# Kernel tuning notes

Hardware: AMD Instinct MI355X
Metric: run time of the kernel (lower is better)

Reference implementation:

```python
import jax, jax.numpy as jnp
import numpy as np

B, N, E = 16, 1024, 32768
HEADS, OC = 4, 8          # GATConv: out_channels = d_out // heads = 8
D_IN, A_DIM = 33, 8
DM, DO = 16, 32
EPS_LN = 1e-5


def setup_inputs() -> dict:
    key = jax.random.key(0)
    ks = jax.random.split(key, 24)
    r = lambda k, s: (0.1 * jax.random.normal(k, s)).astype(jnp.float32)
    return {
        "H": jax.random.normal(ks[0], (B, N, D_IN + A_DIM + 1), dtype=jnp.float32),
        "edge_index": jax.random.randint(ks[1], (2, E), 0, N, dtype=jnp.int32),
        "fc_s_w": r(ks[2], (DM, D_IN)), "fc_s_b": r(ks[3], (DM,)),
        "fc_a_w": r(ks[4], (DM, A_DIM)), "fc_a_b": r(ks[5], (DM,)),
        "fc_r_w": r(ks[6], (DM, 1)), "fc_r_b": r(ks[7], (DM,)),
        "fuse_q": r(ks[8], (3, DM)),
        "fuse_k_w": r(ks[9], (DM, DM)),
        "fuse_v_w": r(ks[10], (DM, DM)),
        "proj_w": r(ks[11], (DO, DM)), "proj_b": r(ks[12], (DO,)),
        "post_w": r(ks[13], (DO, DO)), "post_b": r(ks[14], (DO,)),
        "ln_g": jnp.ones((DO,), jnp.float32), "ln_b": jnp.zeros((DO,), jnp.float32),
        "gat_w": r(ks[15], (HEADS * OC, DO)),
        "att_src": r(ks[16], (HEADS, OC)),
        "att_dst": r(ks[17], (HEADS, OC)),
        "gat_b": r(ks[18], (HEADS * OC,)),
    }


def reference(H, edge_index, fc_s_w, fc_s_b, fc_a_w, fc_a_b, fc_r_w, fc_r_b,
              fuse_q, fuse_k_w, fuse_v_w, proj_w, proj_b, post_w, post_b,
              ln_g, ln_b, gat_w, att_src, att_dst, gat_b):
    # ---- ObsEmbedding: split obs | prev-action | prev-reward, embed to DM ----
    s = H[..., :D_IN]
    a = H[..., D_IN:D_IN + A_DIM]
    rr = H[..., D_IN + A_DIM:]
    tok = jnp.stack([s @ fc_s_w.T + fc_s_b,
                     a @ fc_a_w.T + fc_a_b,
                     rr @ fc_r_w.T + fc_r_b], axis=-2)            # [B,N,3,DM]
    K = tok @ fuse_k_w.T
    V = tok @ fuse_v_w.T
    attn = jnp.einsum('qd,bntd->bnqt', fuse_q, K) / jnp.sqrt(jnp.float32(DM))
    w = jax.nn.softmax(attn, axis=-1)                             # [B,N,3,3]
    fused = jnp.einsum('bnqt,bntd->bnqd', w, V).mean(-2)          # [B,N,DM]
    z = jax.nn.relu(fused) @ proj_w.T + proj_b                    # [B,N,DO]
    h = jax.nn.relu(z @ post_w.T + post_b)
    mu = h.mean(-1, keepdims=True)
    var = ((h - mu) ** 2).mean(-1, keepdims=True)
    Hn = (h - mu) / jnp.sqrt(var + EPS_LN) * ln_g + ln_b          # [B,N,DO]

    # ---- GATConv (eval mode: dropout off, add_self_loops=False) ----
    src, dst = edge_index[0], edge_index[1]
    x = (Hn @ gat_w.T).reshape(B, N, HEADS, OC)                   # [B,N,H,OC]
    a_s = (x * att_src).sum(-1)                                   # [B,N,H]
    a_d = (x * att_dst).sum(-1)
    e = jax.nn.leaky_relu(a_s[:, src] + a_d[:, dst], 0.2)         # [B,E,H]

    def per_graph(e_b, x_b):
        # scatter-softmax over incoming edges of each destination node
        m = jax.ops.segment_max(e_b, dst, num_segments=N)
        ex = jnp.exp(e_b - m[dst])
        den = jax.ops.segment_sum(ex, dst, num_segments=N)
        alpha = ex / den[dst]                                     # [E,H]
        out = jax.ops.segment_sum(alpha[:, :, None] * x_b[src], dst,
                                  num_segments=N)                 # [N,H,OC]
        A = jnp.zeros((HEADS, N, N), jnp.float32).at[:, src, dst].add(alpha.T)
        A = A / jnp.maximum(A.sum(-1, keepdims=True), 1e-9)
        return out.reshape(N, HEADS * OC) + gat_b, A

    out, A = jax.vmap(per_graph)(e, x)                            # [B,N,32], [B,H,N,N]
    return out, A
```

## Files before the change

kernel.cpp:

```cpp
#include <hip/hip_runtime.h>
#include <math.h>

namespace {

constexpr int B = 16, N = 1024, E = 32768, HEADS = 4, OC = 8;
constexpr int D_IN = 33, A_DIM = 8, DM = 16, DO = 32;
constexpr int F = D_IN + A_DIM + 1;
constexpr int BCAP = 256;
constexpr int FILLB = E / 256;
constexpr int ROWS_PER_BLK = 8;

typedef float f4 __attribute__((ext_vector_type(4)));
typedef float f2 __attribute__((ext_vector_type(2)));

__device__ __forceinline__ float lrelu(float x) { return x >= 0.f ? x : 0.2f * x; }


__global__ __launch_bounds__(256) void k_prep(
    const int* __restrict__ ei, int* __restrict__ cnt_src,
    int* __restrict__ cnt_dst, int* __restrict__ bkt_src,
    int* __restrict__ bkt_dst,
    const float* __restrict__ H,
    const float* __restrict__ fc_s_w, const float* __restrict__ fc_s_b,
    const float* __restrict__ fc_a_w, const float* __restrict__ fc_a_b,
    const float* __restrict__ fc_r_w, const float* __restrict__ fc_r_b,
    const float* __restrict__ fuse_q, const float* __restrict__ fuse_k_w,
    const float* __restrict__ fuse_v_w, const float* __restrict__ proj_w,
    const float* __restrict__ proj_b, const float* __restrict__ post_w,
    const float* __restrict__ post_b, const float* __restrict__ ln_g,
    const float* __restrict__ ln_b, const float* __restrict__ gat_w,
    const float* __restrict__ att_src, const float* __restrict__ att_dst,
    float* __restrict__ x_out, float* __restrict__ as_out, float* __restrict__ advi) {
  if (blockIdx.x < FILLB) {
    int e = blockIdx.x * 256 + threadIdx.x;
    int s = ei[e], d = ei[E + e];
    int p1 = atomicAdd(&cnt_src[s], 1);
    if (p1 < BCAP) bkt_src[s * BCAP + p1] = d;
    int p2 = atomicAdd(&cnt_dst[d], 1);
    if (p2 < BCAP) bkt_dst[d * BCAP + p2] = s;
    return;
  }
  int node = (blockIdx.x - FILLB) * 256 + threadIdx.x;
  if (node >= B * N) return;

  const float* hin = H + (size_t)node * F;
  float hv[F];
#pragma unroll
  for (int i = 0; i < F; i++) hv[i] = hin[i];

  float tok[3][DM];
#pragma unroll
  for (int j = 0; j < DM; j++) {
    float acc = fc_s_b[j];
#pragma unroll
    for (int i = 0; i < D_IN; i++) acc = fmaf(hv[i], fc_s_w[j * D_IN + i], acc);
    tok[0][j] = acc;
    float acc2 = fc_a_b[j];
#pragma unroll
    for (int i = 0; i < A_DIM; i++) acc2 = fmaf(hv[D_IN + i], fc_a_w[j * A_DIM + i], acc2);
    tok[1][j] = acc2;
    tok[2][j] = fmaf(hv[F - 1], fc_r_w[j], fc_r_b[j]);
  }

  float Kf[3][DM], Vf[3][DM];
#pragma unroll
  for (int t = 0; t < 3; t++) {
#pragma unroll
    for (int j = 0; j < DM; j++) {
      float ak = 0.f, av = 0.f;
#pragma unroll
      for (int d = 0; d < DM; d++) {
        ak = fmaf(tok[t][d], fuse_k_w[j * DM + d], ak);
        av = fmaf(tok[t][d], fuse_v_w[j * DM + d], av);
      }
      Kf[t][j] = ak; Vf[t][j] = av;
    }
  }

  float wbar[3] = {0.f, 0.f, 0.f};
#pragma unroll
  for (int q = 0; q < 3; q++) {
    float att[3];
#pragma unroll
    for (int t = 0; t < 3; t++) {
      float acc = 0.f;
#pragma unroll
      for (int d = 0; d < DM; d++) acc = fmaf(fuse_q[q * DM + d], Kf[t][d], acc);
      att[t] = acc * 0.25f;
    }
    float mx = fmaxf(att[0], fmaxf(att[1], att[2]));
    float e0 = expf(att[0] - mx), e1 = expf(att[1] - mx), e2 = expf(att[2] - mx);
    float inv = 1.f / (e0 + e1 + e2);
    wbar[0] += e0 * inv; wbar[1] += e1 * inv; wbar[2] += e2 * inv;
  }

  float fused[DM];
#pragma unroll
  for (int d = 0; d < DM; d++) {
    float f = (wbar[0] * Vf[0][d] + wbar[1] * Vf[1][d] + wbar[2] * Vf[2][d]) * (1.f / 3.f);
    fused[d] = fmaxf(f, 0.f);
  }

  float z[DO];
#pragma unroll
  for (int o = 0; o < DO; o++) {
    float acc = proj_b[o];
#pragma unroll
    for (int d = 0; d < DM; d++) acc = fmaf(fused[d], proj_w[o * DM + d], acc);
    z[o] = acc;
  }

  float h2[DO]; float mu = 0.f;
#pragma unroll
  for (int o = 0; o < DO; o++) {
    float acc = post_b[o];
#pragma unroll
    for (int d = 0; d < DO; d++) acc = fmaf(z[d], post_w[o * DO + d], acc);
    acc = fmaxf(acc, 0.f);
    h2[o] = acc; mu += acc;
  }
  mu *= (1.f / DO);
  float var = 0.f;
#pragma unroll
  for (int o = 0; o < DO; o++) { float dd = h2[o] - mu; var = fmaf(dd, dd, var); }
  var *= (1.f / DO);
  float rstd = rsqrtf(var + 1e-5f);
  float Hn[DO];
#pragma unroll
  for (int o = 0; o < DO; o++) Hn[o] = fmaf((h2[o] - mu) * rstd, ln_g[o], ln_b[o]);

  float* xrow = x_out + (size_t)node * (HEADS * OC);
  f4 asv;
#pragma unroll
  for (int hh = 0; hh < HEADS; hh++) {
    float as = 0.f, ad = 0.f;
#pragma unroll
    for (int oc = 0; oc < OC; oc++) {
      int k = hh * OC + oc;
      float acc = 0.f;
#pragma unroll
      for (int d = 0; d < DO; d++) acc = fmaf(Hn[d], gat_w[k * DO + d], acc);
      xrow[k] = acc;
      as = fmaf(acc, att_src[k], as);
      ad = fmaf(acc, att_dst[k], ad);
    }
    asv[hh] = as;
    advi[(size_t)node * 8 + 2 * hh] = ad;
  }
  *(f4*)(as_out + (size_t)node * HEADS) = asv;
}

__global__ __launch_bounds__(256) void k_inv(
    const int* __restrict__ cnt_dst, const int* __restrict__ bkt_dst,
    const float* __restrict__ as_, float* __restrict__ advi) {
  int w = threadIdx.x >> 6, lane = threadIdx.x & 63;
  int r = blockIdx.x * 4 + w;
  int b = r & (B - 1), dn = r >> 4;
  int deg = min(cnt_dst[dn], BCAP);
  const int* list = bkt_dst + dn * BCAP;

  const float* adp = advi + (size_t)(b * N + dn) * 8;
  float a0 = adp[0], a1 = adp[2], a2 = adp[4], a3 = adp[6];

  float sm0 = 0.f, sm1 = 0.f, sm2 = 0.f, sm3 = 0.f;
  for (int i = lane; i < deg; i += 64) {
    int s = list[i];
    f4 ap = *(const f4*)(as_ + (size_t)(b * N + s) * HEADS);
    sm0 += __expf(lrelu(ap.x + a0));
    sm1 += __expf(lrelu(ap.y + a1));
    sm2 += __expf(lrelu(ap.z + a2));
    sm3 += __expf(lrelu(ap.w + a3));
  }
#pragma unroll
  for (int off = 1; off < 64; off <<= 1) {
    sm0 += __shfl_xor(sm0, off);
    sm1 += __shfl_xor(sm1, off);
    sm2 += __shfl_xor(sm2, off);
    sm3 += __shfl_xor(sm3, off);
  }
  if (lane == 0) {
    float* ivp = advi + (size_t)(b * N + dn) * 8 + 1;
    ivp[0] = sm0 > 0.f ? 1.f / sm0 : 0.f;
    ivp[2] = sm1 > 0.f ? 1.f / sm1 : 0.f;
    ivp[4] = sm2 > 0.f ? 1.f / sm2 : 0.f;
    ivp[6] = sm3 > 0.f ? 1.f / sm3 : 0.f;
  }
}

__global__ __launch_bounds__(256) void k_outA(
    const int* __restrict__ cnt_src, const int* __restrict__ bkt_src,
    const int* __restrict__ cnt_dst, const int* __restrict__ bkt_dst,
    const float* __restrict__ as_, const float* __restrict__ advi,
    const float* __restrict__ x_, const float* __restrict__ gat_b,
    float* __restrict__ out, float* __restrict__ A) {
  __shared__ float row[HEADS][N];
  int h = threadIdx.x >> 6, lane = threadIdx.x & 63;
  f4* rowv = (f4*)row[h];

  int r0 = blockIdx.x * ROWS_PER_BLK;
  int s = r0 >> 4;
  int degO = min(cnt_src[s], BCAP);
  const int* listO = bkt_src + s * BCAP;
  int degI = min(cnt_dst[s], BCAP);
  const int* listI = bkt_dst + s * BCAP;
  float gb = gat_b[h * OC + (lane & 7)];

  for (int r = r0; r < r0 + ROWS_PER_BLK; ++r) {
    int b = r & (B - 1);

#pragma unroll
    for (int j = 0; j < 4; j++) rowv[lane + j * 64] = (f4){0.f, 0.f, 0.f, 0.f};
    __syncthreads();

    float as_h = as_[(size_t)(b * N + s) * HEADS + h];
    float rs = 0.f;
    for (int i = lane; i < degO; i += 64) {
      int d = listO[i];
      f2 rec = *(const f2*)(advi + (size_t)(b * N + d) * 8 + 2 * h);
      float a = __expf(lrelu(as_h + rec.x)) * rec.y;
      atomicAdd(&row[h][d], a);
      rs += a;
    }
#pragma unroll
    for (int off = 1; off < 64; off <<= 1) rs += __shfl_xor(rs, off);

    {
      f2 self = *(const f2*)(advi + (size_t)(b * N + s) * 8 + 2 * h);
      int eslot = lane >> 3, cl = lane & 7, c = h * OC + cl;
      float acc = 0.f;
      for (int i = eslot; i < degI; i += 8) {
        int src = listI[i];
        float ex = __expf(lrelu(as_[(size_t)(b * N + src) * HEADS + h] + self.x));
        acc = fmaf(ex, x_[(size_t)(b * N + src) * (HEADS * OC) + c], acc);
      }
      acc += __shfl_xor(acc, 8);
      acc += __shfl_xor(acc, 16);
      acc += __shfl_xor(acc, 32);
      if (eslot == 0)
        out[(size_t)(b * N + s) * (HEADS * OC) + c] = acc * self.y + gb;
    }

    __syncthreads();

    float ivr = 1.f / fmaxf(rs, 1e-9f);
    float* Arow = A + (((size_t)b * HEADS + h) * N + s) * N;
#pragma unroll
    for (int j = 0; j < 4; j++) {
      f4 v = rowv[lane + j * 64];
      v.x *= ivr; v.y *= ivr; v.z *= ivr; v.w *= ivr;
      __builtin_nontemporal_store(v, (f4*)Arow + lane + j * 64);
    }
  }
}

}

extern "C" void kernel_launch(void* const* d_in, const int* in_sizes, int n_in,
                              void* d_out, int out_size, void* d_ws, size_t ws_size,
                              hipStream_t stream) {
  const float* H      = (const float*)d_in[0];
  const int*   ei     = (const int*)  d_in[1];
  const float* fc_s_w = (const float*)d_in[2];
  const float* fc_s_b = (const float*)d_in[3];
  const float* fc_a_w = (const float*)d_in[4];
  const float* fc_a_b = (const float*)d_in[5];
  const float* fc_r_w = (const float*)d_in[6];
  const float* fc_r_b = (const float*)d_in[7];
  const float* fuse_q = (const float*)d_in[8];
  const float* fuse_k_w = (const float*)d_in[9];
  const float* fuse_v_w = (const float*)d_in[10];
  const float* proj_w = (const float*)d_in[11];
  const float* proj_b = (const float*)d_in[12];
  const float* post_w = (const float*)d_in[13];
  const float* post_b = (const float*)d_in[14];
  const float* ln_g   = (const float*)d_in[15];
  const float* ln_b   = (const float*)d_in[16];
  const float* gat_w  = (const float*)d_in[17];
  const float* att_src = (const float*)d_in[18];
  const float* att_dst = (const float*)d_in[19];
  const float* gat_b  = (const float*)d_in[20];

  float* out = (float*)d_out;
  float* A   = out + (size_t)B * N * DO;

  float* ws   = (float*)d_ws;
  float* xbuf = ws;
  float* asb  = xbuf + (size_t)B * N * (HEADS * OC);
  float* advi = asb + (size_t)B * N * HEADS;
  int* ibase   = (int*)(advi + (size_t)B * N * 8);
  int* cnt_src = ibase;
  int* cnt_dst = cnt_src + N;
  int* bkt_src = cnt_dst + N;
  int* bkt_dst = bkt_src + N * BCAP;

  (void)hipMemsetAsync(cnt_src, 0, 2 * N * sizeof(int), stream);
  k_prep<<<dim3(FILLB + (B * N) / 256), dim3(256), 0, stream>>>(
      ei, cnt_src, cnt_dst, bkt_src, bkt_dst,
      H, fc_s_w, fc_s_b, fc_a_w, fc_a_b, fc_r_w, fc_r_b, fuse_q, fuse_k_w,
      fuse_v_w, proj_w, proj_b, post_w, post_b, ln_g, ln_b, gat_w, att_src,
      att_dst, xbuf, asb, advi);

  k_inv<<<dim3(B * N / 4), dim3(256), 0, stream>>>(cnt_dst, bkt_dst, asb, advi);

  k_outA<<<dim3(B * N / ROWS_PER_BLK), dim3(256), 0, stream>>>(
      cnt_src, bkt_src, cnt_dst, bkt_dst, asb, advi, xbuf, gat_b, out, A);
}
```

Before: 106.5 us.

## Split output aggregation into separate blocks and drop block barriers in A-row pass

The final kernel now uses separate block ranges. The first range builds and writes the normalized attention rows A. The extra blocks compute the GAT output aggregation, one wavefront per (batch, node), with 32 channels and 2 edge slots. The __syncthreads calls in the A pass are replaced by s_waitcnt lgkmcnt(0) plus a sched barrier, since each head's row is touched only by its own wavefront. This is meant to shorten the per-row critical path and spread the gather work, at the cost of more blocks and reliance on wave-local LDS ordering.

```diff
diff --git a/kernel.cpp b/kernel.cpp
--- a/kernel.cpp
+++ b/kernel.cpp
@@ -9,6 +9,8 @@
 constexpr int BCAP = 256;
 constexpr int FILLB = E / 256;
 constexpr int ROWS_PER_BLK = 8;
+constexpr int ABLK = B * N / ROWS_PER_BLK;
+constexpr int OUTB = B * N / 4;
 
 typedef float f4 __attribute__((ext_vector_type(4)));
 typedef float f2 __attribute__((ext_vector_type(2)));
@@ -187,70 +189,74 @@
   }
 }
 
-__global__ __launch_bounds__(256) void k_outA(
+__global__ __launch_bounds__(256) void k_final(
     const int* __restrict__ cnt_src, const int* __restrict__ bkt_src,
     const int* __restrict__ cnt_dst, const int* __restrict__ bkt_dst,
     const float* __restrict__ as_, const float* __restrict__ advi,
     const float* __restrict__ x_, const float* __restrict__ gat_b,
     float* __restrict__ out, float* __restrict__ A) {
   __shared__ float row[HEADS][N];
-  int h = threadIdx.x >> 6, lane = threadIdx.x & 63;
-  f4* rowv = (f4*)row[h];
-
-  int r0 = blockIdx.x * ROWS_PER_BLK;
-  int s = r0 >> 4;
-  int degO = min(cnt_src[s], BCAP);
-  const int* listO = bkt_src + s * BCAP;
-  int degI = min(cnt_dst[s], BCAP);
-  const int* listI = bkt_dst + s * BCAP;
-  float gb = gat_b[h * OC + (lane & 7)];
-
-  for (int r = r0; r < r0 + ROWS_PER_BLK; ++r) {
-    int b = r & (B - 1);
-
-#pragma unroll
-    for (int j = 0; j < 4; j++) rowv[lane + j * 64] = (f4){0.f, 0.f, 0.f, 0.f};
-    __syncthreads();
-
-    float as_h = as_[(size_t)(b * N + s) * HEADS + h];
-    float rs = 0.f;
-    for (int i = lane; i < degO; i += 64) {
-      int d = listO[i];
-      f2 rec = *(const f2*)(advi + (size_t)(b * N + d) * 8 + 2 * h);
-      float a = __expf(lrelu(as_h + rec.x)) * rec.y;
-      atomicAdd(&row[h][d], a);
-      rs += a;
+
+  if (blockIdx.x < ABLK) {
+    int h = threadIdx.x >> 6, lane = threadIdx.x & 63;
+    f4* rowv = (f4*)row[h];
+
+    int r0 = blockIdx.x * ROWS_PER_BLK;
+    int s = r0 >> 4;
+    int degO = min(cnt_src[s], BCAP);
+    const int* listO = bkt_src + s * BCAP;
+
+    for (int r = r0; r < r0 + ROWS_PER_BLK; ++r) {
+      int b = r & (B - 1);
+
+#pragma unroll
+      for (int j = 0; j < 4; j++) rowv[lane + j * 64] = (f4){0.f, 0.f, 0.f, 0.f};
+      asm volatile("s_waitcnt lgkmcnt(0)" ::: "memory");
+
+      float as_h = as_[(size_t)(b * N + s) * HEADS + h];
+      float rs = 0.f;
+      for (int i = lane; i < degO; i += 64) {
+        int d = listO[i];
+        f2 rec = *(const f2*)(advi + (size_t)(b * N + d) * 8 + 2 * h);
+        float a = __expf(lrelu(as_h + rec.x)) * rec.y;
+        atomicAdd(&row[h][d], a);
+        rs += a;
+      }
+#pragma unroll
+      for (int off = 1; off < 64; off <<= 1) rs += __shfl_xor(rs, off);
+      asm volatile("s_waitcnt lgkmcnt(0)" ::: "memory");
+      __builtin_amdgcn_sched_barrier(0);
+
+      float ivr = 1.f / fmaxf(rs, 1e-9f);
+      float* Arow = A + (((size_t)b * HEADS + h) * N + s) * N;
+#pragma unroll
+      for (int j = 0; j < 4; j++) {
+        f4 v = rowv[lane + j * 64];
+        v.x *= ivr; v.y *= ivr; v.z *= ivr; v.w *= ivr;
+        __builtin_nontemporal_store(v, (f4*)Arow + lane + j * 64);
+      }
     }
-#pragma unroll
-    for (int off = 1; off < 64; off <<= 1) rs += __shfl_xor(rs, off);
-
-    {
-      f2 self = *(const f2*)(advi + (size_t)(b * N + s) * 8 + 2 * h);
-      int eslot = lane >> 3, cl = lane & 7, c = h * OC + cl;
-      float acc = 0.f;
-      for (int i = eslot; i < degI; i += 8) {
-        int src = listI[i];
-        float ex = __expf(lrelu(as_[(size_t)(b * N + src) * HEADS + h] + self.x));
-        acc = fmaf(ex, x_[(size_t)(b * N + src) * (HEADS * OC) + c], acc);
-      }
-      acc += __shfl_xor(acc, 8);
-      acc += __shfl_xor(acc, 16);
-      acc += __shfl_xor(acc, 32);
-      if (eslot == 0)
-        out[(size_t)(b * N + s) * (HEADS * OC) + c] = acc * self.y + gb;
-    }
-
-    __syncthreads();
-
-    float ivr = 1.f / fmaxf(rs, 1e-9f);
-    float* Arow = A + (((size_t)b * HEADS + h) * N + s) * N;
-#pragma unroll
-    for (int j = 0; j < 4; j++) {
-      f4 v = rowv[lane + j * 64];
-      v.x *= ivr; v.y *= ivr; v.z *= ivr; v.w *= ivr;
-      __builtin_nontemporal_store(v, (f4*)Arow + lane + j * 64);
-    }
-  }
+    return;
+  }
+
+  int w = threadIdx.x >> 6, lane = threadIdx.x & 63;
+  int r = (blockIdx.x - ABLK) * 4 + w;
+  int b = r & (B - 1), dn = r >> 4;
+  int degI = min(cnt_dst[dn], BCAP);
+  const int* listI = bkt_dst + dn * BCAP;
+
+  int c = lane & 31, eslot = lane >> 5;
+  int h3 = c >> 3;
+  f2 self = *(const f2*)(advi + (size_t)(b * N + dn) * 8 + 2 * h3);
+  float acc = 0.f;
+  for (int i = eslot; i < degI; i += 2) {
+    int src = listI[i];
+    float ex = __expf(lrelu(as_[(size_t)(b * N + src) * HEADS + h3] + self.x));
+    acc = fmaf(ex, x_[(size_t)(b * N + src) * (HEADS * OC) + c], acc);
+  }
+  acc += __shfl_xor(acc, 32);
+  if (lane < 32)
+    out[(size_t)(b * N + dn) * (HEADS * OC) + c] = acc * self.y + gat_b[c];
 }
 
 }
@@ -302,6 +308,6 @@
 
   k_inv<<<dim3(B * N / 4), dim3(256), 0, stream>>>(cnt_dst, bkt_dst, asb, advi);
 
-  k_outA<<<dim3(B * N / ROWS_PER_BLK), dim3(256), 0, stream>>>(
+  k_final<<<dim3(ABLK + OUTB), dim3(256), 0, stream>>>(
       cnt_src, bkt_src, cnt_dst, bkt_dst, asb, advi, xbuf, gat_b, out, A);
 }
```

Result: slower. 120.6 us (+13.2%).
